# Optimization experiments

Hardware: AMD Instinct MI355X
Metric: run time of the kernel (lower is better)

The kernel has to match this reference:

```python
import jax, jax.numpy as jnp
import numpy as np

K = 4        # num_kernels
TOPK = 16    # per-row hyperedge sparsification
CHEB_T = 2   # Chebyshev order
ROW_TEMP = 1.0
PI_ITERS = 5  # power-iteration steps


def setup_inputs() -> dict:
    key = jax.random.key(0)
    N, D, D_out = 4096, 256, 256
    ks = jax.random.split(key, 5)
    X = jax.random.normal(ks[0], (N, D), jnp.float32)
    L_k = jax.random.normal(ks[1], (K, D, D), jnp.float32) * 0.02
    alpha = jnp.ones((K,), jnp.float32)
    theta = jax.random.normal(ks[2], (CHEB_T + 1, D), jnp.float32) * 0.02
    rho_raw = jnp.zeros((), jnp.float32)
    proj_w = jax.random.normal(ks[3], (D_out, D), jnp.float32) / np.sqrt(D).astype(np.float32)
    proj_b = jnp.zeros((D_out,), jnp.float32)
    return {"X": X, "L_k": L_k, "alpha": alpha, "theta": theta,
            "rho_raw": rho_raw, "proj_w": proj_w, "proj_b": proj_b}


def reference(X, L_k, alpha, theta, rho_raw, proj_w, proj_b):
    N, D = X.shape
    tau = max(ROW_TEMP, 1e-6)
    # 1) K bilinear kernels: A_k = X L_k X^T / sqrt(D), row-softmax with temp
    A = jnp.einsum('nd,kde,me->knm', X, L_k, X) / jnp.sqrt(jnp.asarray(D, X.dtype))
    H_stack = jax.nn.softmax(A / tau, axis=2)                 # (K, N, N)
    w = jax.nn.softmax(alpha)[:, None, None]
    H_fused = (H_stack * w).sum(0)                            # (N, N)
    # 2) incidence B (N, E=K*N): hyperedge (k,i) holds topk targets of row i of head k
    vals, idx = jax.lax.top_k(H_stack, TOPK)                  # (K, N, TOPK)
    vals = vals / (vals.sum(-1, keepdims=True) + 1e-9)
    E = K * N
    cols = jnp.arange(K)[:, None, None] * N + jnp.arange(N)[None, :, None]
    cols = jnp.broadcast_to(cols, (K, N, TOPK)).reshape(-1)
    rows = idx.reshape(-1)
    B = jnp.zeros((N, E), X.dtype).at[rows, cols].set(vals.reshape(-1))
    W = jnp.ones((E,), X.dtype)
    # 3) normalized hypergraph Laplacian L = I - Dv^{-1/2} B W De^{-1} B^T Dv^{-1/2}
    De = B.sum(0) + 1e-9                                      # (E,)
    Dv = (B * W[None, :]).sum(1) + 1e-9                       # (N,)
    Dv_is = jnp.sqrt(1.0 / Dv)
    S = (B * (W / De)[None, :]) @ B.T                         # (N, N)
    S_norm = Dv_is[:, None] * S * Dv_is[None, :]
    I = jnp.eye(N, dtype=X.dtype)
    L = I - S_norm
    # 4) lambda_max via power iteration on detached L (constant w.r.t. grads)
    Ld = jax.lax.stop_gradient(L)
    v = jax.random.normal(jax.random.key(1), (N, 1), X.dtype)
    v = v / (jnp.linalg.norm(v) + 1e-9)
    for _ in range(PI_ITERS):
        v = Ld @ v
        v = v / (jnp.linalg.norm(v) + 1e-9)
    lam = jnp.clip((v.T @ (Ld @ v)).squeeze(), 1e-3, None)
    lam = jax.lax.stop_gradient(lam)
    L_tilde = (2.0 / lam) * L - I
    # Chebyshev recursion: sum_t T_t(L_tilde) X * theta_t, then ELU
    T0 = X
    out = T0 * theta[0][None, :]
    T1 = L_tilde @ X
    out = out + T1 * theta[1][None, :]
    for t in range(2, CHEB_T + 1):
        T2 = 2.0 * (L_tilde @ T1) - T0
        out = out + T2 * theta[t][None, :]
        T0, T1 = T1, T2
    Z_spec = jax.nn.elu(out)
    # 5) residual blend with kernel diffusion
    Z_kern = H_fused @ X
    rho = jax.nn.sigmoid(rho_raw)
    Z_mix = rho * Z_spec + (1.0 - rho) * Z_kern
    # 6) final projection
    return Z_mix @ proj_w.T + proj_b
```

## Files before the change

### kernel.cpp

```cpp
#include <hip/hip_runtime.h>

typedef unsigned short u16;
typedef unsigned long long u64;
typedef _Float16 h16;
typedef __attribute__((ext_vector_type(8))) _Float16 h16x8;
typedef __attribute__((ext_vector_type(4))) _Float16 h16x4;
typedef __attribute__((ext_vector_type(4))) float f32x4;

__device__ __forceinline__ float b2f(u16 u) {
  unsigned x = ((unsigned)u) << 16;
  return __uint_as_float(x);
}
__device__ __forceinline__ unsigned fkey(float f) {
  unsigned b = __float_as_uint(f);
  return (b & 0x80000000u) ? ~b : (b | 0x80000000u);
}
__device__ __forceinline__ float unfkey(unsigned u) {
  unsigned b = (u & 0x80000000u) ? (u ^ 0x80000000u) : ~u;
  return __uint_as_float(b);
}
__device__ __forceinline__ f32x4 mfma16(h16x8 a, h16x8 b, f32x4 c) {
  return __builtin_amdgcn_mfma_f32_16x16x32_f16(a, b, c, 0, 0, 0);
}
__device__ __forceinline__ void gl_lds16(const void* g, void* l) {
  __builtin_amdgcn_global_load_lds(
      (const __attribute__((address_space(1))) unsigned*)g,
      (__attribute__((address_space(3))) unsigned*)l, 16, 0, 0);
}
__device__ __forceinline__ u64 wave_max_u64(u64 k) {
#pragma unroll
  for (int off = 32; off; off >>= 1) {
    u64 o = __shfl_xor(k, off);
    if (o > k) k = o;
  }
  return k;
}

__global__ void detect_dtype(const u16* __restrict__ X, int* __restrict__ flag) {
  __shared__ int cnt;
  if (threadIdx.x == 0) cnt = 0;
  __syncthreads();
  int sane = 0;
#pragma unroll
  for (int j = 0; j < 16; ++j) {
    u16 u = X[(threadIdx.x * 16 + j) * 2];
    int e = (u >> 7) & 0xff;
    if (u == 0 || (e >= 112 && e <= 142)) sane++;
  }
  atomicAdd(&cnt, sane);
  __syncthreads();
  if (threadIdx.x == 0) *flag = (cnt < 3072) ? 1 : 0;
}

__global__ __launch_bounds__(256) void split_input3(
    const void* __restrict__ in, h16* __restrict__ hi, h16* __restrict__ lo,
    float* __restrict__ f32out, int n, const int* __restrict__ flag) {
  int f = *flag;
  int stride = gridDim.x * 256;
  for (int i = blockIdx.x * 256 + threadIdx.x; i < n; i += stride) {
    float x = f ? ((const float*)in)[i] : b2f(((const u16*)in)[i]);
    h16 h = (h16)x;
    hi[i] = h;
    lo[i] = (h16)(x - (float)h);
    if (f32out) f32out[i] = x;
  }
}

__global__ __launch_bounds__(256) void split_f32h(
    const float* __restrict__ in, h16* __restrict__ hi, h16* __restrict__ lo,
    int n) {
  int stride = gridDim.x * 256;
  for (int i = blockIdx.x * 256 + threadIdx.x; i < n; i += stride) {
    float x = in[i];
    h16 h = (h16)x;
    hi[i] = h;
    lo[i] = (h16)(x - (float)h);
  }
}

__global__ __launch_bounds__(256) void conv_f32(const void* __restrict__ in,
                                                float* __restrict__ out, int n,
                                                const int* __restrict__ flag) {
  int f = *flag;
  int stride = gridDim.x * 256;
  for (int i = blockIdx.x * 256 + threadIdx.x; i < n; i += stride)
    out[i] = f ? ((const float*)in)[i] : b2f(((const u16*)in)[i]);
}

template <bool BIAS>
__global__ __launch_bounds__(256) void gemm3_nt(
    const h16* __restrict__ Ah, const h16* __restrict__ Al,
    const h16* __restrict__ Bh, const h16* __restrict__ Bl,
    float* __restrict__ C, const float* __restrict__ bias, float alpha,
    int M, int Nc, int Kd, long batchA, long batchB, long batchC) {
  const h16* Abh = Ah + (size_t)blockIdx.z * batchA;
  const h16* Abl = Al + (size_t)blockIdx.z * batchA;
  const h16* Bbh = Bh + (size_t)blockIdx.z * batchB;
  const h16* Bbl = Bl + (size_t)blockIdx.z * batchB;
  float* Cb = C + (size_t)blockIdx.z * batchC;
  int bn = blockIdx.x, bm = blockIdx.y;
  int tid = threadIdx.x;
  int wid = tid >> 6, lane = tid & 63;
  __shared__ h16 Ash[64 * 40], Asl[64 * 40], Bsh[64 * 40], Bsl[64 * 40];
  f32x4 acc00 = {}, acc01 = {}, acc10 = {}, acc11 = {};
  int lr = tid >> 2;
  int lc = (tid & 3) << 3;
  size_t aoff = (size_t)(bm * 64 + lr) * Kd + lc;
  size_t boff = (size_t)(bn * 64 + lr) * Kd + lc;
  int wm = (wid & 1) * 32, wn = (wid >> 1) * 32;
  int fr = lane & 15;
  int fc = (lane >> 4) << 3;
  for (int k0 = 0; k0 < Kd; k0 += 32) {
    uint4 avh = *(const uint4*)(Abh + aoff + k0);
    uint4 avl = *(const uint4*)(Abl + aoff + k0);
    uint4 bvh = *(const uint4*)(Bbh + boff + k0);
    uint4 bvl = *(const uint4*)(Bbl + boff + k0);
    __syncthreads();
    *(uint4*)(Ash + lr * 40 + lc) = avh;
    *(uint4*)(Asl + lr * 40 + lc) = avl;
// ... 75 lines not shown
#pragma unroll
    for (int i = 0; i < 4; ++i) {
      int ra = wm + 16 * i + fr;
      int ca = (fcc ^ ((ra >> 1) & 3)) * 8;
      fa[0][i] = *(const h16x8*)(sAh + ra * 32 + ca);
      fa[1][i] = *(const h16x8*)(sAl + ra * 32 + ca);
      int rb = wn + 16 * i + fr;
      int cb = (fcc ^ ((rb >> 1) & 3)) * 8;
      fb[0][i] = *(const h16x8*)(sBh + rb * 32 + cb);
      fb[1][i] = *(const h16x8*)(sBl + rb * 32 + cb);
    }
#pragma unroll
    for (int i = 0; i < 4; ++i)
#pragma unroll
      for (int j = 0; j < 4; ++j) {
        acc[i][j] = mfma16(fa[0][i], fb[0][j], acc[i][j]);
        acc[i][j] = mfma16(fa[0][i], fb[1][j], acc[i][j]);
        acc[i][j] = mfma16(fa[1][i], fb[0][j], acc[i][j]);
      }
  }
  int crow = (lane >> 4) << 2, ccol = lane & 15;
#pragma unroll
  for (int i = 0; i < 4; ++i)
#pragma unroll
    for (int j = 0; j < 4; ++j) {
      int r0 = bm * 128 + wm + 16 * i + crow;
      int c0 = bn * 128 + wn + 16 * j + ccol;
#pragma unroll
      for (int rg = 0; rg < 4; ++rg)
        C[(size_t)(r0 + rg) * Nc + c0] = acc[i][j][rg] * alpha;
    }
}

__global__ __launch_bounds__(256) void gemm_ks(
    const h16* __restrict__ A, const h16* __restrict__ B,
    float* __restrict__ Cpart, int Kd, int Kc) {
  __shared__ h16 sA[128 * 32], sB[128 * 32];
  int tid = threadIdx.x, wid = tid >> 6, lane = tid & 63;
  int bm = blockIdx.y, bn = blockIdx.x, kz = blockIdx.z;
  int kbase = kz * Kc;
  int srow = 32 * wid + (lane >> 2);
  int scnk = lane & 3;
  int fr = lane & 15, fcc = lane >> 4;
  f32x4 acc[4][4] = {};
  int wm = (wid & 1) * 64, wn = (wid >> 1) * 64;
  for (int k0 = 0; k0 < Kc; k0 += 32) {
    __syncthreads();
#pragma unroll
    for (int h = 0; h < 2; ++h) {
      int r = srow + 16 * h;
      int cs = scnk ^ ((r >> 1) & 3);
      size_t goffA = (size_t)(bm * 128 + r) * Kd + kbase + k0 + cs * 8;
      size_t goffB = (size_t)(bn * 128 + r) * Kd + kbase + k0 + cs * 8;
      int loff = (32 * wid + 16 * h) * 32;
      gl_lds16(A + goffA, sA + loff);
      gl_lds16(B + goffB, sB + loff);
    }
    __syncthreads();
    h16x8 fa[4], fb[4];
#pragma unroll
    for (int i = 0; i < 4; ++i) {
      int ra = wm + 16 * i + fr;
      int ca = (fcc ^ ((ra >> 1) & 3)) * 8;
      fa[i] = *(const h16x8*)(sA + ra * 32 + ca);
      int rb = wn + 16 * i + fr;
      int cb = (fcc ^ ((rb >> 1) & 3)) * 8;
      fb[i] = *(const h16x8*)(sB + rb * 32 + cb);
    }
#pragma unroll
    for (int i = 0; i < 4; ++i)
#pragma unroll
      for (int j = 0; j < 4; ++j)
        acc[i][j] = mfma16(fa[i], fb[j], acc[i][j]);
  }
  float* Cp = Cpart + (size_t)kz * 4096 * 256;
  int crow = (lane >> 4) << 2, ccol = lane & 15;
#pragma unroll
  for (int i = 0; i < 4; ++i)
#pragma unroll
    for (int j = 0; j < 4; ++j) {
      int r0 = bm * 128 + wm + 16 * i + crow;
      int c0 = bn * 128 + wn + 16 * j + ccol;
#pragma unroll
      for (int rg = 0; rg < 4; ++rg)
        Cp[(size_t)(r0 + rg) * 256 + c0] = acc[i][j][rg];
    }
}

__global__ __launch_bounds__(256) void ks_reduce(
    const float* __restrict__ Cpart, const float* __restrict__ scptr,
    const float* __restrict__ rowSinv, float* __restrict__ Zk) {
  int i = (blockIdx.x * 256 + threadIdx.x) * 4;
  float4 s = {0.f, 0.f, 0.f, 0.f};
#pragma unroll
  for (int z = 0; z < 8; ++z) {
    float4 p = *(const float4*)(Cpart + (size_t)z * 4096 * 256 + i);
    s.x += p.x; s.y += p.y; s.z += p.z; s.w += p.w;
  }
  float sc = (*scptr) * rowSinv[i >> 8];
  float4 zk = *(float4*)(Zk + i);
  zk.x += sc * s.x; zk.y += sc * s.y; zk.z += sc * s.z; zk.w += sc * s.w;
  *(float4*)(Zk + i) = zk;
}

__global__ __launch_bounds__(256) void transpose16(
    const u16* __restrict__ in, u16* __restrict__ out, int rows, int cols) {
  __shared__ u16 t[32][33];
  const u16* ib = in + (size_t)blockIdx.z * rows * cols;
  u16* ob = out + (size_t)blockIdx.z * rows * cols;
  int r0 = blockIdx.x * 32, c0 = blockIdx.y * 32;
  int tx = threadIdx.x & 31, ty = threadIdx.x >> 5;
#pragma unroll
  for (int i = 0; i < 32; i += 8)
    t[ty + i][tx] = ib[(size_t)(r0 + ty + i) * cols + c0 + tx];
  __syncthreads();
#pragma unroll
  for (int i = 0; i < 32; i += 8)
    ob[(size_t)(c0 + ty + i) * rows + r0 + tx] = t[tx][ty + i];
}

__global__ void prep_scalars(const void* __restrict__ alpha,
                             const void* __restrict__ rho_raw,
                             float* __restrict__ scal,
                             const int* __restrict__ flag) {
  if (threadIdx.x == 0) {
    int f = *flag;
    float a[4], e[4], m = -1e30f, s = 0.f;
    for (int i = 0; i < 4; ++i) {
      a[i] = f ? ((const float*)alpha)[i] : b2f(((const u16*)alpha)[i]);
      m = fmaxf(m, a[i]);
    }
    for (int i = 0; i < 4; ++i) { e[i] = expf(a[i] - m); s += e[i]; }
    for (int i = 0; i < 4; ++i) scal[i] = e[i] / s;
    float rr = f ? ((const float*)rho_raw)[0] : b2f(((const u16*)rho_raw)[0]);
    scal[4] = 1.f / (1.f + expf(-rr));
  }
}

__global__ __launch_bounds__(256) void row_softmax_topk(
    const float* __restrict__ A, float* __restrict__ topv,
    int* __restrict__ topi, h16* __restrict__ E, float* __restrict__ rowSinv,
    int khead) {
  __shared__ u64 candK[4][256];
  __shared__ int candN[4];
  int wid = threadIdx.x >> 6, lane = threadIdx.x & 63;
  int row = blockIdx.x * 4 + wid;
  const float* arow = A + ((size_t)row << 12);
  if (lane == 0) candN[wid] = 0;
  __syncthreads();
  float lm = -INFINITY;
#pragma unroll
  for (int t = 0; t < 16; ++t) {
    float4 v = *(const float4*)(arow + (t << 8) + (lane << 2));
    lm = fmaxf(lm, fmaxf(fmaxf(v.x, v.y), fmaxf(v.z, v.w)));
  }
  float m = lm;
#pragma unroll
  for (int off = 32; off; off >>= 1) m = fmaxf(m, __shfl_xor(m, off));
  u64 lk = ((u64)fkey(lm) << 32) | (unsigned)lane;
  float T = 0.f;
  for (int r = 0; r < 16; ++r) {
    u64 k2 = wave_max_u64(lk);
    if (lk == k2) lk = 0;
    if (r == 15) T = unfkey((unsigned)(k2 >> 32));
  }
  h16* erow = E + ((size_t)row << 12);
  int* cn = &candN[wid];
  u64* ck = candK[wid];
  float s = 0.f;
  for (int t = 0; t < 16; ++t) {
    int c = (t << 8) + (lane << 2);
    float4 v = *(const float4*)(arow + c);
    float e0 = __expf(v.x - m), e1 = __expf(v.y - m);
    float e2 = __expf(v.z - m), e3 = __expf(v.w - m);
    s += (e0 + e1) + (e2 + e3);
    h16x4 hv = {(h16)e0, (h16)e1, (h16)e2, (h16)e3};
    *(h16x4*)(erow + c) = hv;
    if (v.x >= T) {
      int sl = atomicAdd(cn, 1);
      if (sl < 256) ck[sl] = ((u64)fkey(v.x) << 32) | (unsigned)(~(unsigned)c);
    }
    if (v.y >= T) {
      int sl = atomicAdd(cn, 1);
      if (sl < 256) ck[sl] = ((u64)fkey(v.y) << 32) | (unsigned)(~(unsigned)(c + 1));
    }
    if (v.z >= T) {
      int sl = atomicAdd(cn, 1);
      if (sl < 256) ck[sl] = ((u64)fkey(v.z) << 32) | (unsigned)(~(unsigned)(c + 2));
    }
    if (v.w >= T) {
      int sl = atomicAdd(cn, 1);
      if (sl < 256) ck[sl] = ((u64)fkey(v.w) << 32) | (unsigned)(~(unsigned)(c + 3));
    }
  }
#pragma unroll
  for (int off = 32; off; off >>= 1) s += __shfl_xor(s, off);
  if (lane == 0) rowSinv[row] = 1.f / s;
  __syncthreads();
  int cnt = min(*cn, 256);
  u64 loc[4] = {0ull, 0ull, 0ull, 0ull};
  int nl = 0;
  for (int j = lane; j < cnt; j += 64)
    if (nl < 4) loc[nl++] = ck[j];
#define CSW(a, b)                     \
  {                                   \
    if (loc[b] > loc[a]) {            \
      u64 tt = loc[a];                \
      loc[a] = loc[b];                \
      loc[b] = tt;                    \
    }                                 \
  }
  CSW(0, 1) CSW(2, 3) CSW(0, 2) CSW(1, 3) CSW(1, 2)
#undef CSW
  float myv = 0.f;
  int myi = 0;
  float sum16 = 0.f;
  for (int r = 0; r < 16; ++r) {
    u64 key = loc[0];
    u64 k2 = wave_max_u64(key);
    float wv = unfkey((unsigned)(k2 >> 32));
    int wi = (int)(~(unsigned)(k2 & 0xffffffffu));
    if (key == k2 && key != 0ull) {
      loc[0] = loc[1];
      loc[1] = loc[2];
      loc[2] = loc[3];
      loc[3] = 0ull;
    }
    sum16 += expf(wv - m);
    if (r == lane) { myv = wv; myi = wi; }
  }
  if (lane < 16) {
    size_t o = (((size_t)khead << 12) + row) * 16 + lane;
    topv[o] = expf(myv - m) / (sum16 + 1e-9f * s);
    topi[o] = myi;
  }
}

__global__ __launch_bounds__(256) void hist_part(
    const float* __restrict__ topv, const int* __restrict__ topi,
    int* __restrict__ pCnt, float* __restrict__ pDv) {
  __shared__ int lc[4096];
  __shared__ float ld[4096];
  int tid = threadIdx.x, b = blockIdx.x;
  for (int j = tid; j < 4096; j += 256) { lc[j] = 0; ld[j] = 0.f; }
  __syncthreads();
  int base = b * 4096;
#pragma unroll
  for (int j = 0; j < 16; ++j) {
    int t = base + j * 256 + tid;
    atomicAdd(&lc[topi[t]], 1);
    atomicAdd(&ld[topi[t]], topv[t]);
  }
  __syncthreads();
  for (int j = tid; j < 4096; j += 256) {
    pCnt[base + j] = lc[j];
    pDv[base + j] = ld[j];
  }
}

__global__ __launch_bounds__(256) void col_scan(
    const int* __restrict__ pCnt, const float* __restrict__ pDv,
    int* __restrict__ cnt, float* __restrict__ Dvis,
    int* __restrict__ blockBase) {
  int i = blockIdx.x * 256 + threadIdx.x;
  int run = 0;
  float dv = 0.f;
#pragma unroll
  for (int b = 0; b < 64; ++b) {
    blockBase[b * 4096 + i] = run;
    run += pCnt[b * 4096 + i];
    dv += pDv[b * 4096 + i];
  }
  cnt[i] = run;
  Dvis[i] = sqrtf(1.0f / (dv + 1e-9f));
}

__global__ __launch_bounds__(256) void edge_deis(
    const float* __restrict__ topv, float* __restrict__ DeIS) {
  int e = blockIdx.x * 256 + threadIdx.x;
  const float4* p = (const float4*)(topv + ((size_t)e << 4));
  float4 a = p[0], b = p[1], c = p[2], d = p[3];
  float s = ((a.x + a.y) + (a.z + a.w)) + ((b.x + b.y) + (b.z + b.w)) +
            ((c.x + c.y) + (c.z + c.w)) + ((d.x + d.y) + (d.z + d.w));
  DeIS[e] = 1.0f / sqrtf(s + 1e-9f);
}

__global__ __launch_bounds__(256) void scan_rowptr(const int* __restrict__ cnt,
                                                   int* __restrict__ rowptr) {
  __shared__ int part[256];
  int tid = threadIdx.x;
  int base = tid * 16;
  int loc[16];
  int s = 0;
#pragma unroll
  for (int j = 0; j < 16; ++j) { loc[j] = s; s += cnt[base + j]; }
  part[tid] = s;
  __syncthreads();
  for (int off = 1; off < 256; off <<= 1) {
    int v = (tid >= off) ? part[tid - off] : 0;
    __syncthreads();
    part[tid] += v;
    __syncthreads();
  }
  int pre = (tid == 0) ? 0 : part[tid - 1];
#pragma unroll
  for (int j = 0; j < 16; ++j) rowptr[base + j] = pre + loc[j];
  if (tid == 255) rowptr[4096] = part[255];
}

__global__ __launch_bounds__(256) void csr_fill3(
    const float* __restrict__ topv, const int* __restrict__ topi,
    const float* __restrict__ Dvis, const float* __restrict__ DeIS,
    const int* __restrict__ rowptr, const int* __restrict__ blockBase,
    float* __restrict__ cvals, int* __restrict__ colE,
    float* __restrict__ cvalR) {
  __shared__ int lcur[4096];
  int tid = threadIdx.x, b = blockIdx.x;
// ... 9 lines not shown
    float c = Dvis[i] * topv[t] * DeIS[e];
    cvals[t] = c;
    int slot = atomicAdd(&lcur[i], 1);
    colE[slot] = e;
    cvalR[slot] = c;
  }
}

__global__ __launch_bounds__(256) void spmv_edge(
    const float* __restrict__ cvals, const int* __restrict__ topi,
    const float* __restrict__ v, float* __restrict__ g) {
  int e = blockIdx.x * 256 + threadIdx.x;
  float acc = 0.f;
#pragma unroll
  for (int p = 0; p < 16; ++p)
    acc += cvals[e * 16 + p] * v[topi[e * 16 + p]];
  g[e] = acc;
}

__global__ __launch_bounds__(256) void spmv_row(
    const int* __restrict__ rowptr, const int* __restrict__ colE,
    const float* __restrict__ cvalR, const float* __restrict__ g,
    const float* __restrict__ vin, float* __restrict__ vout) {
  int wid = threadIdx.x >> 6, lane = threadIdx.x & 63;
  int row = blockIdx.x * 4 + wid;
  int s = rowptr[row], e = rowptr[row + 1];
  float acc = 0.f;
  for (int j = s + lane; j < e; j += 64) acc += cvalR[j] * g[colE[j]];
#pragma unroll
  for (int off = 32; off; off >>= 1) acc += __shfl_xor(acc, off);
  if (lane == 0) vout[row] = vin[row] - acc;
}

__global__ __launch_bounds__(256) void spmm_edge(
    const float* __restrict__ cvals, const int* __restrict__ topi,
    const float* __restrict__ M, float* __restrict__ G) {
  int wid = threadIdx.x >> 6, lane = threadIdx.x & 63;
  int e = blockIdx.x * 4 + wid;
  int cb = lane << 2;
  const float* cv = cvals + ((size_t)e << 4);
  const int* ti = topi + ((size_t)e << 4);
  float cc[16];
  int ix[16];
#pragma unroll
  for (int p = 0; p < 16; ++p) { cc[p] = cv[p]; ix[p] = ti[p]; }
  float4 acc[4] = {};
#pragma unroll
  for (int h = 0; h < 2; ++h) {
    float4 g[8];
#pragma unroll
    for (int p = 0; p < 8; ++p)
      g[p] = *(const float4*)(M + ((size_t)ix[h * 8 + p] << 8) + cb);
#pragma unroll
    for (int p = 0; p < 8; ++p) {
      float c = cc[h * 8 + p];
      float4 gg = g[p];
      int a = p & 3;
      acc[a].x += c * gg.x; acc[a].y += c * gg.y;
      acc[a].z += c * gg.z; acc[a].w += c * gg.w;
    }
  }
  float4 r;
  r.x = (acc[0].x + acc[1].x) + (acc[2].x + acc[3].x);
  r.y = (acc[0].y + acc[1].y) + (acc[2].y + acc[3].y);
  r.z = (acc[0].z + acc[1].z) + (acc[2].z + acc[3].z);
  r.w = (acc[0].w + acc[1].w) + (acc[2].w + acc[3].w);
  *(float4*)(G + ((size_t)e << 8) + cb) = r;
}

__global__ __launch_bounds__(256) void spmm_row(
    const int* __restrict__ rowptr, const int* __restrict__ colE,
    const float* __restrict__ cvalR, const float* __restrict__ G,
    float* __restrict__ Z) {
  int wid = threadIdx.x >> 6, lane = threadIdx.x & 63;
  int row = blockIdx.x * 4 + wid;
  int cb = lane << 2;
  int s = rowptr[row], e = rowptr[row + 1];
  float4 acc[4] = {};
  int j = s;
  for (; j + 8 <= e; j += 8) {
    int ix[8];
    float cc[8];
#pragma unroll
    for (int t = 0; t < 8; ++t) { ix[t] = colE[j + t]; cc[t] = cvalR[j + t]; }
    float4 g[8];
#pragma unroll
    for (int t = 0; t < 8; ++t)
      g[t] = *(const float4*)(G + ((size_t)ix[t] << 8) + cb);
#pragma unroll
    for (int t = 0; t < 8; ++t) {
      float c = cc[t];
      float4 gg = g[t];
      int a = t & 3;
      acc[a].x += c * gg.x; acc[a].y += c * gg.y;
      acc[a].z += c * gg.z; acc[a].w += c * gg.w;
    }
  }
  for (; j < e; ++j) {
    float c = cvalR[j];
    float4 gg = *(const float4*)(G + ((size_t)colE[j] << 8) + cb);
    acc[0].x += c * gg.x; acc[0].y += c * gg.y;
    acc[0].z += c * gg.z; acc[0].w += c * gg.w;
  }
  float4 r;
  r.x = (acc[0].x + acc[1].x) + (acc[2].x + acc[3].x);
  r.y = (acc[0].y + acc[1].y) + (acc[2].y + acc[3].y);
  r.z = (acc[0].z + acc[1].z) + (acc[2].z + acc[3].z);
  r.w = (acc[0].w + acc[1].w) + (acc[2].w + acc[3].w);
  *(float4*)(Z + ((size_t)row << 8) + cb) = r;
}

__global__ __launch_bounds__(256) void init_v0(float* __restrict__ v) {
  int tid = blockIdx.x * 256 + threadIdx.x;
  unsigned j = (unsigned)(tid & 2047);
  unsigned x0 = j, x1 = j + 2048u;
  const unsigned ks0 = 0u, ks1 = 1u, ks2 = 0x1BD11BDAu;
  x0 += ks0; x1 += ks1;
#define TF_R(r)                                  \
  {                                              \
    x0 += x1;                                    \
    x1 = (x1 << (r)) | (x1 >> (32 - (r)));       \
    x1 ^= x0;                                    \
  }
  TF_R(13) TF_R(15) TF_R(26) TF_R(6)  x0 += ks1; x1 += ks2 + 1u;
  TF_R(17) TF_R(29) TF_R(16) TF_R(24) x0 += ks2; x1 += ks0 + 2u;
  TF_R(13) TF_R(15) TF_R(26) TF_R(6)  x0 += ks0; x1 += ks1 + 3u;
  TF_R(17) TF_R(29) TF_R(16) TF_R(24) x0 += ks1; x1 += ks2 + 4u;
  TF_R(13) TF_R(15) TF_R(26) TF_R(6)  x0 += ks2; x1 += ks0 + 5u;
#undef TF_R
  unsigned bits = (tid < 2048) ? x0 : x1;
  float u01 = __uint_as_float((bits >> 9) | 0x3f800000u) - 1.0f;
  const float lo = -0.99999994f;
  float u = fmaxf(lo, u01 * 2.0f + lo);
  float w = -log1pf(-u * u);
  float p;
  if (w < 5.0f) {
    float t = w - 2.5f;
    p = 2.81022636e-08f;
    p = 3.43273939e-07f + p * t;
    p = -3.5233877e-06f + p * t;
    p = -4.39150654e-06f + p * t;
    p = 0.00021858087f + p * t;
    p = -0.00125372503f + p * t;
    p = -0.00417768164f + p * t;
    p = 0.246640727f + p * t;
    p = 1.50140941f + p * t;
  } else {
    float t = sqrtf(w) - 3.0f;
    p = -0.000200214257f;
    p = 0.000100950558f + p * t;
    p = 0.00134934322f + p * t;
    p = -0.00367342844f + p * t;
    p = 0.00573950773f + p * t;
    p = -0.0076224613f + p * t;
    p = 0.00943887047f + p * t;
    p = 1.00167406f + p * t;
    p = 2.83297682f + p * t;
  }
  v[tid] = 1.41421354f * (p * u);
}

__global__ __launch_bounds__(256) void pi_dots(const float* __restrict__ w5,
                                               const float* __restrict__ w6,
                                               float* __restrict__ scal) {
  __shared__ float r1[256], r2[256];
  int tid = threadIdx.x;
  float a = 0.f, b = 0.f;
  for (int i = tid; i < 4096; i += 256) {
    float x = w5[i];
    a += x * x;
    b += x * w6[i];
  }
  r1[tid] = a; r2[tid] = b;
  __syncthreads();
  for (int off = 128; off; off >>= 1) {
    if (tid < off) { r1[tid] += r1[tid + off]; r2[tid] += r2[tid + off]; }
    __syncthreads();
  }
  if (tid == 0) scal[5] = fmaxf(r2[0] / r1[0], 1e-3f);
}

__global__ __launch_bounds__(256) void t1_simple(
    const float* __restrict__ SnX, const float* __restrict__ Xf,
    const float* __restrict__ scal, float* __restrict__ T1) {
  int i = blockIdx.x * 256 + threadIdx.x;
  float c1 = 2.0f / scal[5];
  T1[i] = (c1 - 1.0f) * Xf[i] - c1 * SnX[i];
}

__global__ __launch_bounds__(256) void combine_kernel(
    const float* __restrict__ Xf, const float* __restrict__ T1,
    const float* __restrict__ SnT1, const float* __restrict__ Zk,
    const float* __restrict__ thetaf, const float* __restrict__ scal,
    h16* __restrict__ Zmh, h16* __restrict__ Zml) {
  int idx = blockIdx.x * 256 + threadIdx.x;
  int d = idx & 255;
  float c1 = 2.0f / scal[5];
  float rho = scal[4];
  float x = Xf[idx];
  float t1 = T1[idx];
  float t2 = 2.0f * ((c1 - 1.0f) * t1 - c1 * SnT1[idx]) - x;
  float o = x * thetaf[d] + t1 * thetaf[256 + d] + t2 * thetaf[512 + d];
  float zs = o > 0.0f ? o : expm1f(o);
  float zm = rho * zs + (1.0f - rho) * Zk[idx];
  h16 h = (h16)zm;
  Zmh[idx] = h;
  Zml[idx] = (h16)(zm - (float)h);
}

extern "C" void kernel_launch(void* const* d_in, const int* in_sizes, int n_in,
                              void* d_out, int out_size, void* d_ws,
                              size_t ws_size, hipStream_t stream) {
  (void)in_sizes; (void)n_in; (void)out_size;
  const void* Xin = d_in[0];
  const void* Lin = d_in[1];
  const void* alpha = d_in[2];
  const void* theta = d_in[3];
  const void* rho_raw = d_in[4];
  const void* Wpin = d_in[5];
  const void* bpin = d_in[6];
  float* out = (float*)d_out;

  char* base = (char*)d_ws;
  size_t off = 0;
  auto alloc = [&](size_t bytes) -> char* {
    char* p = base + off;
    off += (bytes + 255) & ~(size_t)255;
    return p;
  };
  float* Abuf = (float*)alloc((size_t)4096 * 4096 * 4);
  h16* Ebuf = (h16*)alloc((size_t)4096 * 4096 * 2);
  h16* Yhi = (h16*)alloc((size_t)4 * 4096 * 256 * 2);
  h16* Ylo = (h16*)alloc((size_t)4 * 4096 * 256 * 2);
  h16* Xhi = (h16*)alloc((size_t)4096 * 256 * 2);
  h16* Xlo = (h16*)alloc((size_t)4096 * 256 * 2);
  float* Xf = (float*)alloc((size_t)4096 * 256 * 4);
  h16* XT = (h16*)alloc((size_t)256 * 4096 * 2);
  h16* Lhi = (h16*)alloc((size_t)4 * 256 * 256 * 2);
  h16* Llo = (h16*)alloc((size_t)4 * 256 * 256 * 2);
  h16* LThi = (h16*)alloc((size_t)4 * 256 * 256 * 2);
  h16* LTlo = (h16*)alloc((size_t)4 * 256 * 256 * 2);
  h16* Whi = (h16*)alloc((size_t)256 * 256 * 2);
  h16* Wlo = (h16*)alloc((size_t)256 * 256 * 2);
  float* Zk = (float*)alloc((size_t)4096 * 256 * 4);
  float* SnX = (float*)alloc((size_t)4096 * 256 * 4);
  float* T1 = (float*)alloc((size_t)4096 * 256 * 4);
  h16* Zmh = (h16*)alloc((size_t)4096 * 256 * 2);
  h16* Zml = (h16*)alloc((size_t)4096 * 256 * 2);
  float* topv = (float*)alloc((size_t)4 * 4096 * 16 * 4);
  int* topi = (int*)alloc((size_t)4 * 4096 * 16 * 4);
  float* cvals = (float*)alloc((size_t)262144 * 4);
  int* colE = (int*)alloc((size_t)262144 * 4);
  float* cvalR = (float*)alloc((size_t)262144 * 4);
  int* pCnt = (int*)alloc((size_t)64 * 4096 * 4);
  float* pDv = (float*)alloc((size_t)64 * 4096 * 4);
  int* blockBase = (int*)alloc((size_t)64 * 4096 * 4);
  int* rowptr = (int*)alloc(4097 * 4);
  int* cnt = (int*)alloc(4096 * 4);
  float* Dvis = (float*)alloc(4096 * 4);
  float* DeIS = (float*)alloc(16384 * 4);
  float* gE = (float*)alloc(16384 * 4);
  float* wA = (float*)alloc(4096 * 4);
  float* wB = (float*)alloc(4096 * 4);
  float* rowSinv = (float*)alloc(4096 * 4);
  float* thetaf = (float*)alloc(768 * 4);
  float* biasf = (float*)alloc(256 * 4);
  float* scal = (float*)alloc(256);
  int* flag = (int*)alloc(256);
  if (off > ws_size) return;
  float* Yf = (float*)Ebuf;
  float* G = (float*)Abuf;
  float* Kpart = Abuf;

  detect_dtype<<<1, 256, 0, stream>>>((const u16*)Xin, flag);
  split_input3<<<1024, 256, 0, stream>>>(Xin, Xhi, Xlo, Xf, 4096 * 256, flag);
  split_input3<<<256, 256, 0, stream>>>(Lin, Lhi, Llo, nullptr, 4 * 256 * 256,
                                        flag);
  split_input3<<<64, 256, 0, stream>>>(Wpin, Whi, Wlo, nullptr, 256 * 256, flag);
  conv_f32<<<1, 256, 0, stream>>>(theta, thetaf, 768, flag);
  conv_f32<<<1, 256, 0, stream>>>(bpin, biasf, 256, flag);
  prep_scalars<<<1, 64, 0, stream>>>(alpha, rho_raw, scal, flag);
  transpose16<<<dim3(128, 8, 1), 256, 0, stream>>>((const u16*)Xhi, (u16*)XT,
                                                   4096, 256);
  transpose16<<<dim3(8, 8, 4), 256, 0, stream>>>((const u16*)Lhi, (u16*)LThi,
                                                 256, 256);
  transpose16<<<dim3(8, 8, 4), 256, 0, stream>>>((const u16*)Llo, (u16*)LTlo,
                                                 256, 256);
  gemm3_nt<false><<<dim3(4, 64, 4), 256, 0, stream>>>(
      Xhi, Xlo, LThi, LTlo, Yf, nullptr, 1.0f, 4096, 256, 256,
      0L, 256L * 256L, 4096L * 256L);
  split_f32h<<<2048, 256, 0, stream>>>(Yf, Yhi, Ylo, 4 * 4096 * 256);
  hipMemsetAsync(Zk, 0, (size_t)4096 * 256 * 4, stream);
  for (int k = 0; k < 4; ++k) {
    gemm3_big<<<dim3(32, 32), 256, 0, stream>>>(
        Yhi + (size_t)k * 4096 * 256, Ylo + (size_t)k * 4096 * 256, Xhi, Xlo,
        Abuf, 0.0625f, 4096, 4096, 256);
    row_softmax_topk<<<1024, 256, 0, stream>>>(Abuf, topv, topi, Ebuf, rowSinv,
                                               k);
    gemm_ks<<<dim3(2, 32, 8), 256, 0, stream>>>(Ebuf, XT, Kpart, 4096, 512);
    ks_reduce<<<1024, 256, 0, stream>>>(Kpart, scal + k, rowSinv, Zk);
  }
  hist_part<<<64, 256, 0, stream>>>(topv, topi, pCnt, pDv);
  col_scan<<<16, 256, 0, stream>>>(pCnt, pDv, cnt, Dvis, blockBase);
  edge_deis<<<64, 256, 0, stream>>>(topv, DeIS);
  scan_rowptr<<<1, 256, 0, stream>>>(cnt, rowptr);
  csr_fill3<<<64, 256, 0, stream>>>(topv, topi, Dvis, DeIS, rowptr, blockBase,
                                    cvals, colE, cvalR);
  init_v0<<<16, 256, 0, stream>>>(wA);
  for (int it = 0; it < 6; ++it) {
    const float* vi = (it & 1) ? wB : wA;
    float* vo = (it & 1) ? wA : wB;
    spmv_edge<<<64, 256, 0, stream>>>(cvals, topi, vi, gE);
    spmv_row<<<1024, 256, 0, stream>>>(rowptr, colE, cvalR, gE, vi, vo);
  }
  pi_dots<<<1, 256, 0, stream>>>(wB, wA, scal);
  spmm_edge<<<4096, 256, 0, stream>>>(cvals, topi, Xf, G);
  spmm_row<<<1024, 256, 0, stream>>>(rowptr, colE, cvalR, G, SnX);
  t1_simple<<<4096, 256, 0, stream>>>(SnX, Xf, scal, T1);
  spmm_edge<<<4096, 256, 0, stream>>>(cvals, topi, T1, G);
  spmm_row<<<1024, 256, 0, stream>>>(rowptr, colE, cvalR, G, SnX);
  combine_kernel<<<4096, 256, 0, stream>>>(Xf, T1, SnX, Zk, thetaf, scal, Zmh,
                                           Zml);
  gemm3_nt<true><<<dim3(4, 64, 1), 256, 0, stream>>>(
      Zmh, Zml, Whi, Wlo, out, biasf, 1.0f, 4096, 256, 256, 0L, 0L, 0L);
}
```

Baseline: 717.9 us.

## Batch kernel-diffusion GEMM across heads and fuse small prep and epilogue kernels

Stores all four heads' dense softmax matrices in one larger buffer. The per-head split-K GEMM plus reduce then becomes a single 4-head launch with one reduction that writes Zk directly, so the memset is no longer needed. Several small kernels are merged to cut launch count: the L/W input splits, the theta/bias/scalar prep, edge degrees into hist_part, v0 init into col_scan, and the T1 and combine epilogues into the SpMM row kernel. The trade-off is a much larger workspace (64M halves for E) and more memory traffic for the batched E matrix.

Result: faster. 675.3 us (median of 2 runs) (-5.9%).

```diff
diff --git a/kernel.cpp b/kernel.cpp
--- a/kernel.cpp
+++ b/kernel.cpp
@@ -35,6 +35,9 @@
   }
   return k;
 }
+__device__ __forceinline__ float cvt_in(const void* p, int i, int f) {
+  return f ? ((const float*)p)[i] : b2f(((const u16*)p)[i]);
+}
 
 __global__ void detect_dtype(const u16* __restrict__ X, int* __restrict__ flag) {
   __shared__ int cnt;
@@ -58,11 +61,39 @@
   int f = *flag;
   int stride = gridDim.x * 256;
   for (int i = blockIdx.x * 256 + threadIdx.x; i < n; i += stride) {
-    float x = f ? ((const float*)in)[i] : b2f(((const u16*)in)[i]);
+    float x = cvt_in(in, i, f);
     h16 h = (h16)x;
     hi[i] = h;
     lo[i] = (h16)(x - (float)h);
     if (f32out) f32out[i] = x;
+  }
+}
+
+__global__ __launch_bounds__(256) void split_LW(
+    const void* __restrict__ Lin, h16* __restrict__ Lhi, h16* __restrict__ Llo,
+    const void* __restrict__ Win, h16* __restrict__ Whi, h16* __restrict__ Wlo,
+    const int* __restrict__ flag) {
+  int f = *flag;
+  int tid = threadIdx.x;
+  if (blockIdx.x < 256) {
+#pragma unroll
+    for (int j = 0; j < 4; ++j) {
+      int i = blockIdx.x * 1024 + j * 256 + tid;
+      float x = cvt_in(Lin, i, f);
+      h16 h = (h16)x;
+      Lhi[i] = h;
+      Llo[i] = (h16)(x - (float)h);
+    }
+  } else {
+    int b = blockIdx.x - 256;
+#pragma unroll
+    for (int j = 0; j < 4; ++j) {
+      int i = b * 1024 + j * 256 + tid;
+      float x = cvt_in(Win, i, f);
+      h16 h = (h16)x;
+      Whi[i] = h;
+      Wlo[i] = (h16)(x - (float)h);
+    }
   }
 }
 
@@ -78,13 +109,28 @@
   }
 }
 
-__global__ __launch_bounds__(256) void conv_f32(const void* __restrict__ in,
-                                                float* __restrict__ out, int n,
-                                                const int* __restrict__ flag) {
+__global__ __launch_bounds__(1024) void prep_small(
+    const void* __restrict__ theta, const void* __restrict__ bpin,
+    const void* __restrict__ alpha, const void* __restrict__ rho_raw,
+    float* __restrict__ thetaf, float* __restrict__ biasf,
+    float* __restrict__ scal, const int* __restrict__ flag) {
   int f = *flag;
-  int stride = gridDim.x * 256;
-  for (int i = blockIdx.x * 256 + threadIdx.x; i < n; i += stride)
-    out[i] = f ? ((const float*)in)[i] : b2f(((const u16*)in)[i]);
+  int tid = threadIdx.x;
+  if (tid < 768)
+    thetaf[tid] = cvt_in(theta, tid, f);
+  else
+    biasf[tid - 768] = cvt_in(bpin, tid - 768, f);
+  if (tid == 0) {
+    float a[4], e[4], m = -1e30f, s = 0.f;
+    for (int i = 0; i < 4; ++i) {
+      a[i] = cvt_in(alpha, i, f);
+      m = fmaxf(m, a[i]);
+    }
+    for (int i = 0; i < 4; ++i) { e[i] = expf(a[i] - m); s += e[i]; }
+    for (int i = 0; i < 4; ++i) scal[i] = e[i] / s;
+    float rr = cvt_in(rho_raw, 0, f);
+    scal[4] = 1.f / (1.f + expf(-rr));
+  }
 }
 
 template <bool BIAS>
@@ -226,26 +272,28 @@
     }
 }
 
-__global__ __launch_bounds__(256) void gemm_ks(
-    const h16* __restrict__ A, const h16* __restrict__ B,
-    float* __restrict__ Cpart, int Kd, int Kc) {
+__global__ __launch_bounds__(256) void gemm_ks4(
+    const h16* __restrict__ Eall, const h16* __restrict__ B,
+    float* __restrict__ Cpart) {
   __shared__ h16 sA[128 * 32], sB[128 * 32];
   int tid = threadIdx.x, wid = tid >> 6, lane = tid & 63;
-  int bm = blockIdx.y, bn = blockIdx.x, kz = blockIdx.z;
-  int kbase = kz * Kc;
+  int bm = blockIdx.y, bn = blockIdx.x, zz = blockIdx.z;
+  int head = zz >> 2, kz = zz & 3;
+  const h16* A = Eall + (size_t)head * 4096 * 4096;
+  int kbase = kz * 1024;
   int srow = 32 * wid + (lane >> 2);
   int scnk = lane & 3;
   int fr = lane & 15, fcc = lane >> 4;
   f32x4 acc[4][4] = {};
   int wm = (wid & 1) * 64, wn = (wid >> 1) * 64;
-  for (int k0 = 0; k0 < Kc; k0 += 32) {
+  for (int k0 = 0; k0 < 1024; k0 += 32) {
     __syncthreads();
 #pragma unroll
     for (int h = 0; h < 2; ++h) {
       int r = srow + 16 * h;
       int cs = scnk ^ ((r >> 1) & 3);
-      size_t goffA = (size_t)(bm * 128 + r) * Kd + kbase + k0 + cs * 8;
-      size_t goffB = (size_t)(bn * 128 + r) * Kd + kbase + k0 + cs * 8;
+      size_t goffA = (size_t)(bm * 128 + r) * 4096 + kbase + k0 + cs * 8;
+      size_t goffB = (size_t)(bn * 128 + r) * 4096 + kbase + k0 + cs * 8;
       int loff = (32 * wid + 16 * h) * 32;
       gl_lds16(A + goffA, sA + loff);
       gl_lds16(B + goffB, sB + loff);
@@ -267,7 +315,7 @@
       for (int j = 0; j < 4; ++j)
         acc[i][j] = mfma16(fa[i], fb[j], acc[i][j]);
   }
-  float* Cp = Cpart + (size_t)kz * 4096 * 256;
+  float* Cp = Cpart + (size_t)zz * 4096 * 256;
   int crow = (lane >> 4) << 2, ccol = lane & 15;
 #pragma unroll
   for (int i = 0; i < 4; ++i)
@@ -281,20 +329,25 @@
     }
 }
 
-__global__ __launch_bounds__(256) void ks_reduce(
-    const float* __restrict__ Cpart, const float* __restrict__ scptr,
+__global__ __launch_bounds__(256) void ks_reduce4(
+    const float* __restrict__ Cpart, const float* __restrict__ scal,
     const float* __restrict__ rowSinv, float* __restrict__ Zk) {
   int i = (blockIdx.x * 256 + threadIdx.x) * 4;
-  float4 s = {0.f, 0.f, 0.f, 0.f};
-#pragma unroll
-  for (int z = 0; z < 8; ++z) {
-    float4 p = *(const float4*)(Cpart + (size_t)z * 4096 * 256 + i);
-    s.x += p.x; s.y += p.y; s.z += p.z; s.w += p.w;
-  }
-  float sc = (*scptr) * rowSinv[i >> 8];
-  float4 zk = *(float4*)(Zk + i);
-  zk.x += sc * s.x; zk.y += sc * s.y; zk.z += sc * s.z; zk.w += sc * s.w;
-  *(float4*)(Zk + i) = zk;
+  int row = i >> 8;
+  float4 out = {0.f, 0.f, 0.f, 0.f};
+#pragma unroll
+  for (int k = 0; k < 4; ++k) {
+    float4 s = {0.f, 0.f, 0.f, 0.f};
+#pragma unroll
+    for (int z = 0; z < 4; ++z) {
+      float4 p = *(const float4*)(Cpart + (size_t)(k * 4 + z) * 4096 * 256 + i);
+      s.x += p.x; s.y += p.y; s.z += p.z; s.w += p.w;
+    }
+    float sc = scal[k] * rowSinv[k * 4096 + row];
+    out.x += sc * s.x; out.y += sc * s.y;
+    out.z += sc * s.z; out.w += sc * s.w;
+  }
+  *(float4*)(Zk + i) = out;
 }
 
 __global__ __launch_bounds__(256) void transpose16(
@@ -313,27 +366,9 @@
     ob[(size_t)(c0 + ty + i) * rows + r0 + tx] = t[tx][ty + i];
 }
 
-__global__ void prep_scalars(const void* __restrict__ alpha,
-                             const void* __restrict__ rho_raw,
-                             float* __restrict__ scal,
-                             const int* __restrict__ flag) {
-  if (threadIdx.x == 0) {
-    int f = *flag;
-    float a[4], e[4], m = -1e30f, s = 0.f;
-    for (int i = 0; i < 4; ++i) {
-      a[i] = f ? ((const float*)alpha)[i] : b2f(((const u16*)alpha)[i]);
-      m = fmaxf(m, a[i]);
-    }
-    for (int i = 0; i < 4; ++i) { e[i] = expf(a[i] - m); s += e[i]; }
-    for (int i = 0; i < 4; ++i) scal[i] = e[i] / s;
-    float rr = f ? ((const float*)rho_raw)[0] : b2f(((const u16*)rho_raw)[0]);
-    scal[4] = 1.f / (1.f + expf(-rr));
-  }
-}
-
 __global__ __launch_bounds__(256) void row_softmax_topk(
     const float* __restrict__ A, float* __restrict__ topv,
-    int* __restrict__ topi, h16* __restrict__ E, float* __restrict__ rowSinv,
+    int* __restrict__ topi, h16* __restrict__ E, float* __restrict__ rowSinvK,
     int khead) {
   __shared__ u64 candK[4][256];
   __shared__ int candN[4];
@@ -389,7 +424,7 @@
   }
 #pragma unroll
   for (int off = 32; off; off >>= 1) s += __shfl_xor(s, off);
-  if (lane == 0) rowSinv[row] = 1.f / s;
+  if (lane == 0) rowSinvK[row] = 1.f / s;
   __syncthreads();
   int cnt = min(*cn, 256);
   u64 loc[4] = {0ull, 0ull, 0ull, 0ull};
@@ -432,7 +467,8 @@
 
 __global__ __launch_bounds__(256) void hist_part(
     const float* __restrict__ topv, const int* __restrict__ topi,
-    int* __restrict__ pCnt, float* __restrict__ pDv) {
+    int* __restrict__ pCnt, float* __restrict__ pDv,
+    float* __restrict__ DeIS) {
   __shared__ int lc[4096];
   __shared__ float ld[4096];
   int tid = threadIdx.x, b = blockIdx.x;
@@ -450,12 +486,18 @@
     pCnt[base + j] = lc[j];
     pDv[base + j] = ld[j];
   }
+  int e = b * 256 + tid;
+  const float4* p = (const float4*)(topv + ((size_t)e << 4));
+  float4 a = p[0], bb = p[1], c = p[2], d = p[3];
+  float s = ((a.x + a.y) + (a.z + a.w)) + ((bb.x + bb.y) + (bb.z + bb.w)) +
+            ((c.x + c.y) + (c.z + c.w)) + ((d.x + d.y) + (d.z + d.w));
+  DeIS[e] = 1.0f / sqrtf(s + 1e-9f);
 }
 
 __global__ __launch_bounds__(256) void col_scan(
     const int* __restrict__ pCnt, const float* __restrict__ pDv,
     int* __restrict__ cnt, float* __restrict__ Dvis,
-    int* __restrict__ blockBase) {
+    int* __restrict__ blockBase, float* __restrict__ v0) {
   int i = blockIdx.x * 256 + threadIdx.x;
   int run = 0;
   float dv = 0.f;
@@ -467,16 +509,55 @@
   }
   cnt[i] = run;
   Dvis[i] = sqrtf(1.0f / (dv + 1e-9f));
-}
-
-__global__ __launch_bounds__(256) void edge_deis(
-    const float* __restrict__ topv, float* __restrict__ DeIS) {
-  int e = blockIdx.x * 256 + threadIdx.x;
-  const float4* p = (const float4*)(topv + ((size_t)e << 4));
-  float4 a = p[0], b = p[1], c = p[2], d = p[3];
-  float s = ((a.x + a.y) + (a.z + a.w)) + ((b.x + b.y) + (b.z + b.w)) +
-            ((c.x + c.y) + (c.z + c.w)) + ((d.x + d.y) + (d.z + d.w));
-  DeIS[e] = 1.0f / sqrtf(s + 1e-9f);
+  {
+    int tid = i;
+    unsigned j = (unsigned)(tid & 2047);
+    unsigned x0 = j, x1 = j + 2048u;
+    const unsigned ks0 = 0u, ks1 = 1u, ks2 = 0x1BD11BDAu;
+#define TF_R(r)                                \
+    {                                          \
+      x0 += x1;                                \
+      x1 = (x1 << (r)) | (x1 >> (32 - (r)));   \
+      x1 ^= x0;                                \
+    }
+    x0 += ks0; x1 += ks1;
+    TF_R(13) TF_R(15) TF_R(26) TF_R(6)  x0 += ks1; x1 += ks2 + 1u;
+    TF_R(17) TF_R(29) TF_R(16) TF_R(24) x0 += ks2; x1 += ks0 + 2u;
+    TF_R(13) TF_R(15) TF_R(26) TF_R(6)  x0 += ks0; x1 += ks1 + 3u;
+    TF_R(17) TF_R(29) TF_R(16) TF_R(24) x0 += ks1; x1 += ks2 + 4u;
+    TF_R(13) TF_R(15) TF_R(26) TF_R(6)  x0 += ks2; x1 += ks0 + 5u;
+#undef TF_R
+    unsigned bits = (tid < 2048) ? x0 : x1;
+    float u01 = __uint_as_float((bits >> 9) | 0x3f800000u) - 1.0f;
+    const float lo = -0.99999994f;
+    float u = fmaxf(lo, u01 * 2.0f + lo);
+    float w = -log1pf(-u * u);
+    float p;
+    if (w < 5.0f) {
+      float t = w - 2.5f;
+      p = 2.81022636e-08f;
+      p = 3.43273939e-07f + p * t;
+      p = -3.5233877e-06f + p * t;
+      p = -4.39150654e-06f + p * t;
+      p = 0.00021858087f + p * t;
+      p = -0.00125372503f + p * t;
+      p = -0.00417768164f + p * t;
+      p = 0.246640727f + p * t;
+      p = 1.50140941f + p * t;
+    } else {
+      float t = sqrtf(w) - 3.0f;
+      p = -0.000200214257f;
+      p = 0.000100950558f + p * t;
+      p = 0.00134934322f + p * t;
+      p = -0.00367342844f + p * t;
+      p = 0.00573950773f + p * t;
+      p = -0.0076224613f + p * t;
+      p = 0.00943887047f + p * t;
+      p = 1.00167406f + p * t;
+      p = 2.83297682f + p * t;
+    }
+    v0[tid] = 1.41421354f * (p * u);
+  }
 }
 
 __global__ __launch_bounds__(256) void scan_rowptr(const int* __restrict__ cnt,
@@ -552,6 +633,26 @@
   if (lane == 0) vout[row] = vin[row] - acc;
 }
 
+__global__ __launch_bounds__(256) void pi_dots(const float* __restrict__ w5,
+                                               const float* __restrict__ w6,
+                                               float* __restrict__ scal) {
+  __shared__ float r1[256], r2[256];
+  int tid = threadIdx.x;
+  float a = 0.f, b = 0.f;
+  for (int i = tid; i < 4096; i += 256) {
+    float x = w5[i];
+    a += x * x;
+    b += x * w6[i];
+  }
+  r1[tid] = a; r2[tid] = b;
+  __syncthreads();
+  for (int off = 128; off; off >>= 1) {
+    if (tid < off) { r1[tid] += r1[tid + off]; r2[tid] += r2[tid + off]; }
+    __syncthreads();
+  }
+  if (tid == 0) scal[5] = fmaxf(r2[0] / r1[0], 1e-3f);
+}
+
 __global__ __launch_bounds__(256) void spmm_edge(
     const float* __restrict__ cvals, const int* __restrict__ topi,
     const float* __restrict__ M, float* __restrict__ G) {
@@ -588,10 +689,14 @@
   *(float4*)(G + ((size_t)e << 8) + cb) = r;
 }
 
-__global__ __launch_bounds__(256) void spmm_row(
+template <int MODE>
+__global__ __launch_bounds__(256) void spmm_row_ep(
     const int* __restrict__ rowptr, const int* __restrict__ colE,
     const float* __restrict__ cvalR, const float* __restrict__ G,
-    float* __restrict__ Z) {
+    const float* __restrict__ Xf, float* __restrict__ T1,
+    const float* __restrict__ Zk, const float* __restrict__ thetaf,
+    const float* __restrict__ scal, h16* __restrict__ Zmh,
+    h16* __restrict__ Zml) {
   int wid = threadIdx.x >> 6, lane = threadIdx.x & 63;
   int row = blockIdx.x * 4 + wid;
   int cb = lane << 2;
@@ -622,110 +727,41 @@
     acc[0].x += c * gg.x; acc[0].y += c * gg.y;
     acc[0].z += c * gg.z; acc[0].w += c * gg.w;
   }
-  float4 r;
-  r.x = (acc[0].x + acc[1].x) + (acc[2].x + acc[3].x);
-  r.y = (acc[0].y + acc[1].y) + (acc[2].y + acc[3].y);
-  r.z = (acc[0].z + acc[1].z) + (acc[2].z + acc[3].z);
-  r.w = (acc[0].w + acc[1].w) + (acc[2].w + acc[3].w);
-  *(float4*)(Z + ((size_t)row << 8) + cb) = r;
-}
-
-__global__ __launch_bounds__(256) void init_v0(float* __restrict__ v) {
-  int tid = blockIdx.x * 256 + threadIdx.x;
-  unsigned j = (unsigned)(tid & 2047);
-  unsigned x0 = j, x1 = j + 2048u;
-  const unsigned ks0 = 0u, ks1 = 1u, ks2 = 0x1BD11BDAu;
-  x0 += ks0; x1 += ks1;
-#define TF_R(r)                                  \
-  {                                              \
-    x0 += x1;                                    \
-    x1 = (x1 << (r)) | (x1 >> (32 - (r)));       \
-    x1 ^= x0;                                    \
-  }
-  TF_R(13) TF_R(15) TF_R(26) TF_R(6)  x0 += ks1; x1 += ks2 + 1u;
-  TF_R(17) TF_R(29) TF_R(16) TF_R(24) x0 += ks2; x1 += ks0 + 2u;
-  TF_R(13) TF_R(15) TF_R(26) TF_R(6)  x0 += ks0; x1 += ks1 + 3u;
-  TF_R(17) TF_R(29) TF_R(16) TF_R(24) x0 += ks1; x1 += ks2 + 4u;
-  TF_R(13) TF_R(15) TF_R(26) TF_R(6)  x0 += ks2; x1 += ks0 + 5u;
-#undef TF_R
-  unsigned bits = (tid < 2048) ? x0 : x1;
-  float u01 = __uint_as_float((bits >> 9) | 0x3f800000u) - 1.0f;
-  const float lo = -0.99999994f;
-  float u = fmaxf(lo, u01 * 2.0f + lo);
-  float w = -log1pf(-u * u);
-  float p;
-  if (w < 5.0f) {
-    float t = w - 2.5f;
-    p = 2.81022636e-08f;
-    p = 3.43273939e-07f + p * t;
-    p = -3.5233877e-06f + p * t;
-    p = -4.39150654e-06f + p * t;
-    p = 0.00021858087f + p * t;
-    p = -0.00125372503f + p * t;
-    p = -0.00417768164f + p * t;
-    p = 0.246640727f + p * t;
-    p = 1.50140941f + p * t;
+  float4 z;
+  z.x = (acc[0].x + acc[1].x) + (acc[2].x + acc[3].x);
+  z.y = (acc[0].y + acc[1].y) + (acc[2].y + acc[3].y);
+  z.z = (acc[0].z + acc[1].z) + (acc[2].z + acc[3].z);
+  z.w = (acc[0].w + acc[1].w) + (acc[2].w + acc[3].w);
+  size_t o = ((size_t)row << 8) + cb;
+  float c1 = 2.0f / scal[5];
+  float4 x = *(const float4*)(Xf + o);
+  if constexpr (MODE == 1) {
+    float4 t1;
+    t1.x = (c1 - 1.0f) * x.x - c1 * z.x;
+    t1.y = (c1 - 1.0f) * x.y - c1 * z.y;
+    t1.z = (c1 - 1.0f) * x.z - c1 * z.z;
+    t1.w = (c1 - 1.0f) * x.w - c1 * z.w;
+    *(float4*)(T1 + o) = t1;
   } else {
-    float t = sqrtf(w) - 3.0f;
-    p = -0.000200214257f;
-    p = 0.000100950558f + p * t;
-    p = 0.00134934322f + p * t;
-    p = -0.00367342844f + p * t;
-    p = 0.00573950773f + p * t;
-    p = -0.0076224613f + p * t;
-    p = 0.00943887047f + p * t;
-    p = 1.00167406f + p * t;
-    p = 2.83297682f + p * t;
-  }
-  v[tid] = 1.41421354f * (p * u);
-}
-
-__global__ __launch_bounds__(256) void pi_dots(const float* __restrict__ w5,
-                                               const float* __restrict__ w6,
-                                               float* __restrict__ scal) {
-  __shared__ float r1[256], r2[256];
-  int tid = threadIdx.x;
-  float a = 0.f, b = 0.f;
-  for (int i = tid; i < 4096; i += 256) {
-    float x = w5[i];
-    a += x * x;
-    b += x * w6[i];
-  }
-  r1[tid] = a; r2[tid] = b;
-  __syncthreads();
-  for (int off = 128; off; off >>= 1) {
-    if (tid < off) { r1[tid] += r1[tid + off]; r2[tid] += r2[tid + off]; }
-    __syncthreads();
-  }
-  if (tid == 0) scal[5] = fmaxf(r2[0] / r1[0], 1e-3f);
-}
-
-__global__ __launch_bounds__(256) void t1_simple(
-    const float* __restrict__ SnX, const float* __restrict__ Xf,
-    const float* __restrict__ scal, float* __restrict__ T1) {
-  int i = blockIdx.x * 256 + threadIdx.x;
-  float c1 = 2.0f / scal[5];
-  T1[i] = (c1 - 1.0f) * Xf[i] - c1 * SnX[i];
-}
-
-__global__ __launch_bounds__(256) void combine_kernel(
-    const float* __restrict__ Xf, const float* __restrict__ T1,
-    const float* __restrict__ SnT1, const float* __restrict__ Zk,
-    const float* __restrict__ thetaf, const float* __restrict__ scal,
-    h16* __restrict__ Zmh, h16* __restrict__ Zml) {
-  int idx = blockIdx.x * 256 + threadIdx.x;
-  int d = idx & 255;
-  float c1 = 2.0f / scal[5];
-  float rho = scal[4];
-  float x = Xf[idx];
-  float t1 = T1[idx];
-  float t2 = 2.0f * ((c1 - 1.0f) * t1 - c1 * SnT1[idx]) - x;
-  float o = x * thetaf[d] + t1 * thetaf[256 + d] + t2 * thetaf[512 + d];
-  float zs = o > 0.0f ? o : expm1f(o);
-  float zm = rho * zs + (1.0f - rho) * Zk[idx];
-  h16 h = (h16)zm;
-  Zmh[idx] = h;
-  Zml[idx] = (h16)(zm - (float)h);
+    float rho = scal[4];
+    float4 t1 = *(const float4*)(T1 + o);
+    float4 zk = *(const float4*)(Zk + o);
+    h16x4 hh, hl;
+#pragma unroll
+    for (int q = 0; q < 4; ++q) {
+      float xv = (&x.x)[q], t1v = (&t1.x)[q], zv = (&z.x)[q], zkv = (&zk.x)[q];
+      int d = cb + q;
+      float t2 = 2.0f * ((c1 - 1.0f) * t1v - c1 * zv) - xv;
+      float oo = xv * thetaf[d] + t1v * thetaf[256 + d] + t2 * thetaf[512 + d];
+      float zs = oo > 0.0f ? oo : expm1f(oo);
+      float zm = rho * zs + (1.0f - rho) * zkv;
+      h16 h = (h16)zm;
+      hh[q] = h;
+      hl[q] = (h16)(zm - (float)h);
+    }
+    *(h16x4*)(Zmh + o) = hh;
+    *(h16x4*)(Zml + o) = hl;
+  }
 }
 
 extern "C" void kernel_launch(void* const* d_in, const int* in_sizes, int n_in,
@@ -749,7 +785,7 @@
     return p;
   };
   float* Abuf = (float*)alloc((size_t)4096 * 4096 * 4);
-  h16* Ebuf = (h16*)alloc((size_t)4096 * 4096 * 2);
+  h16* Eall = (h16*)alloc((size_t)4 * 4096 * 4096 * 2);
   h16* Yhi = (h16*)alloc((size_t)4 * 4096 * 256 * 2);
   h16* Ylo = (h16*)alloc((size_t)4 * 4096 * 256 * 2);
   h16* Xhi = (h16*)alloc((size_t)4096 * 256 * 2);
@@ -763,7 +799,6 @@
   h16* Whi = (h16*)alloc((size_t)256 * 256 * 2);
   h16* Wlo = (h16*)alloc((size_t)256 * 256 * 2);
   float* Zk = (float*)alloc((size_t)4096 * 256 * 4);
-  float* SnX = (float*)alloc((size_t)4096 * 256 * 4);
   float* T1 = (float*)alloc((size_t)4096 * 256 * 4);
   h16* Zmh = (h16*)alloc((size_t)4096 * 256 * 2);
   h16* Zml = (h16*)alloc((size_t)4096 * 256 * 2);
@@ -782,24 +817,21 @@
   float* gE = (float*)alloc(16384 * 4);
   float* wA = (float*)alloc(4096 * 4);
   float* wB = (float*)alloc(4096 * 4);
-  float* rowSinv = (float*)alloc(4096 * 4);
+  float* rowSinv = (float*)alloc((size_t)4 * 4096 * 4);
   float* thetaf = (float*)alloc(768 * 4);
   float* biasf = (float*)alloc(256 * 4);
   float* scal = (float*)alloc(256);
   int* flag = (int*)alloc(256);
   if (off > ws_size) return;
-  float* Yf = (float*)Ebuf;
+  float* Yf = (float*)Eall;
+  float* Kpart = Abuf;
   float* G = (float*)Abuf;
-  float* Kpart = Abuf;
 
   detect_dtype<<<1, 256, 0, stream>>>((const u16*)Xin, flag);
   split_input3<<<1024, 256, 0, stream>>>(Xin, Xhi, Xlo, Xf, 4096 * 256, flag);
-  split_input3<<<256, 256, 0, stream>>>(Lin, Lhi, Llo, nullptr, 4 * 256 * 256,
-                                        flag);
-  split_input3<<<64, 256, 0, stream>>>(Wpin, Whi, Wlo, nullptr, 256 * 256, flag);
-  conv_f32<<<1, 256, 0, stream>>>(theta, thetaf, 768, flag);
-  conv_f32<<<1, 256, 0, stream>>>(bpin, biasf, 256, flag);
-  prep_scalars<<<1, 64, 0, stream>>>(alpha, rho_raw, scal, flag);
+  split_LW<<<320, 256, 0, stream>>>(Lin, Lhi, Llo, Wpin, Whi, Wlo, flag);
+  prep_small<<<1, 1024, 0, stream>>>(theta, bpin, alpha, rho_raw, thetaf, biasf,
+                                     scal, flag);
   transpose16<<<dim3(128, 8, 1), 256, 0, stream>>>((const u16*)Xhi, (u16*)XT,
                                                    4096, 256);
   transpose16<<<dim3(8, 8, 4), 256, 0, stream>>>((const u16*)Lhi, (u16*)LThi,
@@ -810,23 +842,21 @@
       Xhi, Xlo, LThi, LTlo, Yf, nullptr, 1.0f, 4096, 256, 256,
       0L, 256L * 256L, 4096L * 256L);
   split_f32h<<<2048, 256, 0, stream>>>(Yf, Yhi, Ylo, 4 * 4096 * 256);
-  hipMemsetAsync(Zk, 0, (size_t)4096 * 256 * 4, stream);
   for (int k = 0; k < 4; ++k) {
     gemm3_big<<<dim3(32, 32), 256, 0, stream>>>(
         Yhi + (size_t)k * 4096 * 256, Ylo + (size_t)k * 4096 * 256, Xhi, Xlo,
         Abuf, 0.0625f, 4096, 4096, 256);
-    row_softmax_topk<<<1024, 256, 0, stream>>>(Abuf, topv, topi, Ebuf, rowSinv,
-                                               k);
-    gemm_ks<<<dim3(2, 32, 8), 256, 0, stream>>>(Ebuf, XT, Kpart, 4096, 512);
-    ks_reduce<<<1024, 256, 0, stream>>>(Kpart, scal + k, rowSinv, Zk);
-  }
-  hist_part<<<64, 256, 0, stream>>>(topv, topi, pCnt, pDv);
-  col_scan<<<16, 256, 0, stream>>>(pCnt, pDv, cnt, Dvis, blockBase);
-  edge_deis<<<64, 256, 0, stream>>>(topv, DeIS);
+    row_softmax_topk<<<1024, 256, 0, stream>>>(
+        Abuf, topv, topi, Eall + (size_t)k * 4096 * 4096, rowSinv + k * 4096,
+        k);
+  }
+  gemm_ks4<<<dim3(2, 32, 16), 256, 0, stream>>>(Eall, XT, Kpart);
+  ks_reduce4<<<1024, 256, 0, stream>>>(Kpart, scal, rowSinv, Zk);
+  hist_part<<<64, 256, 0, stream>>>(topv, topi, pCnt, pDv, DeIS);
+  col_scan<<<16, 256, 0, stream>>>(pCnt, pDv, cnt, Dvis, blockBase, wA);
   scan_rowptr<<<1, 256, 0, stream>>>(cnt, rowptr);
   csr_fill3<<<64, 256, 0, stream>>>(topv, topi, Dvis, DeIS, rowptr, blockBase,
                                     cvals, colE, cvalR);
-  init_v0<<<16, 256, 0, stream>>>(wA);
   for (int it = 0; it < 6; ++it) {
     const float* vi = (it & 1) ? wB : wA;
     float* vo = (it & 1) ? wA : wB;
@@ -835,12 +865,12 @@
   }
   pi_dots<<<1, 256, 0, stream>>>(wB, wA, scal);
   spmm_edge<<<4096, 256, 0, stream>>>(cvals, topi, Xf, G);
-  spmm_row<<<1024, 256, 0, stream>>>(rowptr, colE, cvalR, G, SnX);
-  t1_simple<<<4096, 256, 0, stream>>>(SnX, Xf, scal, T1);
+  spmm_row_ep<1><<<1024, 256, 0, stream>>>(rowptr, colE, cvalR, G, Xf, T1,
+                                           nullptr, thetaf, scal, nullptr,
+                                           nullptr);
   spmm_edge<<<4096, 256, 0, stream>>>(cvals, topi, T1, G);
-  spmm_row<<<1024, 256, 0, stream>>>(rowptr, colE, cvalR, G, SnX);
-  combine_kernel<<<4096, 256, 0, stream>>>(Xf, T1, SnX, Zk, thetaf, scal, Zmh,
-                                           Zml);
+  spmm_row_ep<2><<<1024, 256, 0, stream>>>(rowptr, colE, cvalR, G, Xf, T1, Zk,
+                                           thetaf, scal, Zmh, Zml);
   gemm3_nt<true><<<dim3(4, 64, 1), 256, 0, stream>>>(
       Zmh, Zml, Whi, Wlo, out, biasf, 1.0f, 4096, 256, 256, 0L, 0L, 0L);
 }
```
